# Optimization experiments

Measured on AMD Instinct MI355X. Metric: run time of the kernel, lower is better.

The kernel has to match this reference:

```python
import jax, jax.numpy as jnp
import numpy as np

V, D, L, H, T = 32000, 1024, 4, 16, 1024
DH = D // H
SCALE = DH ** -0.5
FF = 4 * D
R = 2  # n_rounds


def setup_inputs() -> dict:
    key = jax.random.key(0)
    ks = iter(jax.random.split(key, 32))
    s = 0.02
    nrm = lambda shape: jax.random.normal(next(ks), shape, dtype=jnp.float32) * s
    inp = {
        "x": jax.random.randint(next(ks), (2, T), 0, V),
        "embed": nrm((V, D)),
        "pos_embed": nrm((T, D)),
        "Wqkv": nrm((L, R, 3 * D, D)),
        "bqkv": jnp.zeros((L, R, 3 * D), jnp.float32),
        "Wo": nrm((L, D, D)),
        "bo": jnp.zeros((L, D), jnp.float32),
        "Wg": nrm((L, D, 2 * D)),
        "bg": jnp.zeros((L, D), jnp.float32),
        "ln1_g": jnp.ones((L, D), jnp.float32),
        "ln1_b": jnp.zeros((L, D), jnp.float32),
        "W1": nrm((L, FF, D)),
        "b1": jnp.zeros((L, FF), jnp.float32),
        "W2": nrm((L, D, FF)),
        "b2": jnp.zeros((L, D), jnp.float32),
        "ln2_g": jnp.ones((L, D), jnp.float32),
        "ln2_b": jnp.zeros((L, D), jnp.float32),
        "lnf_g": jnp.ones((D,), jnp.float32),
        "lnf_b": jnp.zeros((D,), jnp.float32),
    }
    return inp


def _ln(h, g, b, eps=1e-5):
    m = jnp.mean(h, axis=-1, keepdims=True)
    v = jnp.mean((h - m) ** 2, axis=-1, keepdims=True)
    return (h - m) * jax.lax.rsqrt(v + eps) * g + b


def _attend(h, W, b, mask):
    B, Tq, _ = h.shape
    qkv = (h @ W.T + b).reshape(B, Tq, 3, H, DH)
    q, k, v = qkv[:, :, 0], qkv[:, :, 1], qkv[:, :, 2]  # [B,T,H,DH]
    scores = jnp.einsum("bqhd,bkhd->bhqk", q, k) * SCALE
    scores = jnp.where(mask, scores, -jnp.inf)
    a = jax.nn.softmax(scores, axis=-1)
    return jnp.einsum("bhqk,bkhd->bqhd", a, v).reshape(B, Tq, D)


def reference(x, embed, pos_embed, Wqkv, bqkv, Wo, bo, Wg, bg,
              ln1_g, ln1_b, W1, b1, W2, b2, ln2_g, ln2_b, lnf_g, lnf_b):
    B, Tq = x.shape
    mask = jnp.tril(jnp.ones((Tq, Tq), dtype=bool))
    h = embed[x] + pos_embed[jnp.arange(Tq)]
    for l in range(L):
        n1 = _ln(h, ln1_g[l], ln1_b[l])
        pred = _attend(n1, Wqkv[l, 0], bqkv[l, 0], mask)
        cum = pred
        out = pred
        # boosted round 2: attend on residual, gate the correction
        corr = _attend(n1 - cum, Wqkv[l, 1], bqkv[l, 1], mask)
        gate = jax.nn.sigmoid(jnp.concatenate([cum, corr], axis=-1) @ Wg[l].T + bg[l])
        gated = gate * corr
        out = out + gated
        h = h + (out @ Wo[l].T + bo[l])
        n2 = _ln(h, ln2_g[l], ln2_b[l])
        ff = jax.nn.gelu(n2 @ W1[l].T + b1[l], approximate=False) @ W2[l].T + b2[l]
        h = h + ff
    return _ln(h, lnf_g, lnf_b) @ embed.T  # tied head, no bias
```

## Files before the change

### kernel.cpp

```cpp
#include <hip/hip_runtime.h>
#include <math.h>

#define D_  1024
#define T_  1024
#define B_  2
#define H_  16
#define DH_ 64
#define L_  4
#define FF_ 4096
#define V_  32000
#define M_  2048

typedef _Float16 f16;
typedef _Float16 f16x8 __attribute__((ext_vector_type(8)));
typedef _Float16 f16x4 __attribute__((ext_vector_type(4)));
typedef float    fx4  __attribute__((ext_vector_type(4)));

__global__ __launch_bounds__(256) void f2h_k(const float* __restrict__ in, f16* __restrict__ out) {
    const long i = ((long)blockIdx.x * 256 + threadIdx.x) * 4;
    const float4 v = *(const float4*)(in + i);
    f16x4 o = { (f16)v.x, (f16)v.y, (f16)v.z, (f16)v.w };
    *(f16x4*)(out + i) = o;
}

__global__ __launch_bounds__(256) void embed_k(const int* __restrict__ x, const float* __restrict__ emb,
                                               const float* __restrict__ pos, float* __restrict__ h) {
    const long m = blockIdx.x;
    const int  t = threadIdx.x;
    const long tok = x[m];
    const long pt  = m & (T_ - 1);
    const float4 e = ((const float4*)(emb + tok * D_))[t];
    const float4 p = ((const float4*)(pos + pt * D_))[t];
    ((float4*)(h + m * D_))[t] = make_float4(e.x + p.x, e.y + p.y, e.z + p.z, e.w + p.w);
}

__global__ __launch_bounds__(256) void ln_k(const float* __restrict__ x, const float* __restrict__ g,
                                            const float* __restrict__ b, float* __restrict__ of,
                                            f16* __restrict__ oh) {
    const long m = blockIdx.x;
    const int  t = threadIdx.x;
    const int  wave = t >> 6, lane = t & 63;
    __shared__ float red1[4], red2[4];
    const float4 v = ((const float4*)(x + m * D_))[t];
    float s = v.x + v.y + v.z + v.w;
#pragma unroll
    for (int off = 32; off; off >>= 1) s += __shfl_xor(s, off, 64);
    if (lane == 0) red1[wave] = s;
    __syncthreads();
    const float mean = (red1[0] + red1[1] + red1[2] + red1[3]) * (1.0f / 1024.0f);
    const float d0 = v.x - mean, d1 = v.y - mean, d2 = v.z - mean, d3 = v.w - mean;
    float s2 = d0 * d0 + d1 * d1 + d2 * d2 + d3 * d3;
#pragma unroll
    for (int off = 32; off; off >>= 1) s2 += __shfl_xor(s2, off, 64);
    if (lane == 0) red2[wave] = s2;
    __syncthreads();
    const float var  = (red2[0] + red2[1] + red2[2] + red2[3]) * (1.0f / 1024.0f);
    const float rstd = rsqrtf(var + 1e-5f);
    const float4 gv = ((const float4*)g)[t];
    const float4 bv = ((const float4*)b)[t];
    const float o0 = d0 * rstd * gv.x + bv.x;
    const float o1 = d1 * rstd * gv.y + bv.y;
    const float o2 = d2 * rstd * gv.z + bv.z;
    const float o3 = d3 * rstd * gv.w + bv.w;
    if (of) ((float4*)(of + m * D_))[t] = make_float4(o0, o1, o2, o3);
    if (oh) { f16x4 o = { (f16)o0, (f16)o1, (f16)o2, (f16)o3 }; *(f16x4*)(oh + m * D_ + t * 4) = o; }
}

__global__ __launch_bounds__(256) void sub_k(const float* __restrict__ a, const float* __restrict__ b,
                                             f16* __restrict__ o) {
    const long i = ((long)blockIdx.x * 256 + threadIdx.x) * 4;
    const float4 va = *(const float4*)(a + i);
    const float4 vb = *(const float4*)(b + i);
    f16x4 o4 = { (f16)(va.x - vb.x), (f16)(va.y - vb.y), (f16)(va.z - vb.z), (f16)(va.w - vb.w) };
    *(f16x4*)(o + i) = o4;
}

__global__ __launch_bounds__(256) void cat_k(const float* __restrict__ p, const float* __restrict__ c,
                                             f16* __restrict__ o) {
    const long i = ((long)blockIdx.x * 256 + threadIdx.x) * 4;
    const long m = i >> 11;
    const int  j = (int)(i & 2047);
    const float* src = (j < 1024) ? (p + m * 1024 + j) : (c + m * 1024 + (j - 1024));
    const float4 v = *(const float4*)src;
    f16x4 o4 = { (f16)v.x, (f16)v.y, (f16)v.z, (f16)v.w };
    *(f16x4*)(o + i) = o4;
}

__global__ __launch_bounds__(256) void gate_k(const float* __restrict__ p, const float* __restrict__ c,
                                              const float* __restrict__ gl, f16* __restrict__ o) {
    const long i = ((long)blockIdx.x * 256 + threadIdx.x) * 4;
    const float4 vp = *(const float4*)(p + i);
    const float4 vc = *(const float4*)(c + i);
    const float4 vg = *(const float4*)(gl + i);
    const float s0 = 1.0f / (1.0f + __expf(-vg.x));
    const float s1 = 1.0f / (1.0f + __expf(-vg.y));
    const float s2 = 1.0f / (1.0f + __expf(-vg.z));
    const float s3 = 1.0f / (1.0f + __expf(-vg.w));
    f16x4 o4 = { (f16)(vp.x + s0 * vc.x), (f16)(vp.y + s1 * vc.y),
                 (f16)(vp.z + s2 * vc.z), (f16)(vp.w + s3 * vc.w) };
    *(f16x4*)(o + i) = o4;
}

template<int BN>
__global__ __launch_bounds__(256)
void gemm_bt(const f16* __restrict__ A, const f16* __restrict__ Wt,
             const float* __restrict__ bias, const float* __restrict__ resid,
             float* __restrict__ Cf, f16* __restrict__ Ch,
             int N, int K, int gelu) {
    __shared__ __align__(16) f16 As[3][128 * 32];
    __shared__ __align__(16) f16 Bs[3][BN * 32];
    const int tid  = threadIdx.x;
    const int wave = tid >> 6;
    const int lane = tid & 63;

    const int nbm = gridDim.y;
    const int nbn = gridDim.x;
    int bi = blockIdx.y * nbn + blockIdx.x;
    const int nwg = nbm * nbn;
    if ((nwg & 7) == 0) bi = (bi & 7) * (nwg >> 3) + (bi >> 3);
    const long bm = bi % nbm;
    const long bn = bi / nbm;

    const int wm = (wave >> 1) * 64;
    const int wn = (wave & 1) * (BN / 2);
    constexpr int NJ = BN / 32;

    fx4 acc[4][NJ] = {};

    const int c0 = wave * 2;
    const int r0 = c0 * 16 + (lane >> 2);
    const int cc = (lane & 3) * 8;
    const f16* a0 = A + ((long)bm * 128 + r0) * K + cc;
    const f16* a1 = A + ((long)bm * 128 + r0 + 16) * K + cc;

    const f16* b0;
    const f16* b1 = nullptr;
    if constexpr (BN == 128) {
        b0 = Wt + ((long)bn * 128 + r0) * K + cc;
        b1 = Wt + ((long)bn * 128 + r0 + 16) * K + cc;
    } else {
        b0 = Wt + ((long)bn * 64 + wave * 16 + (lane >> 2)) * K + cc;
    }

    const int NT = K >> 5;

    auto STAGE = [&](int kt) {
        const int k0 = kt * 32;
        const int bf3 = kt % 3;
        __builtin_amdgcn_global_load_lds((const __attribute__((address_space(1))) void*)(a0 + k0),
                                         (__attribute__((address_space(3))) void*)&As[bf3][c0 * 512], 16, 0, 0);
        __builtin_amdgcn_global_load_lds((const __attribute__((address_space(1))) void*)(a1 + k0),
                                         (__attribute__((address_space(3))) void*)&As[bf3][(c0 + 1) * 512], 16, 0, 0);
        if constexpr (BN == 128) {
            __builtin_amdgcn_global_load_lds((const __attribute__((address_space(1))) void*)(b0 + k0),
                                             (__attribute__((address_space(3))) void*)&Bs[bf3][c0 * 512], 16, 0, 0);
            __builtin_amdgcn_global_load_lds((const __attribute__((address_space(1))) void*)(b1 + k0),
                                             (__attribute__((address_space(3))) void*)&Bs[bf3][(c0 + 1) * 512], 16, 0, 0);
        } else {
            __builtin_amdgcn_global_load_lds((const __attribute__((address_space(1))) void*)(b0 + k0),
                                             (__attribute__((address_space(3))) void*)&Bs[bf3][wave * 512], 16, 0, 0);
        }
    };

    STAGE(0);
    if (NT > 1) STAGE(1);

    const int koff = (lane >> 4) * 8;
    for (int t = 0; t < NT; ++t) {
        if (t + 2 < NT) STAGE(t + 2);
        const int rem = NT - 1 - t;
        if constexpr (BN == 128) {
            if (rem >= 2)      asm volatile("s_waitcnt vmcnt(8)" ::: "memory");
            else if (rem == 1) asm volatile("s_waitcnt vmcnt(4)" ::: "memory");
            else               asm volatile("s_waitcnt vmcnt(0)" ::: "memory");
        } else {
            if (rem >= 2)      asm volatile("s_waitcnt vmcnt(6)" ::: "memory");
            else if (rem == 1) asm volatile("s_waitcnt vmcnt(3)" ::: "memory");
            else               asm volatile("s_waitcnt vmcnt(0)" ::: "memory");
        }
        __builtin_amdgcn_s_barrier();
        __builtin_amdgcn_sched_barrier(0);

        const f16* as = As[t % 3];
        const f16* bs = Bs[t % 3];
        f16x8 af[4], bf[NJ];
#pragma unroll
        for (int i = 0; i < 4; ++i)
            af[i] = *(const f16x8*)&as[(wm + i * 16 + (lane & 15)) * 32 + koff];
#pragma unroll
        for (int j = 0; j < NJ; ++j)
            bf[j] = *(const f16x8*)&bs[(wn + j * 16 + (lane & 15)) * 32 + koff];
#pragma unroll
        for (int i = 0; i < 4; ++i)
#pragma unroll
            for (int j = 0; j < NJ; ++j)
                acc[i][j] = __builtin_amdgcn_mfma_f32_16x16x32_f16(af[i], bf[j], acc[i][j], 0, 0, 0);

        asm volatile("s_waitcnt lgkmcnt(0)" ::: "memory");
        __builtin_amdgcn_sched_barrier(0);
        __builtin_amdgcn_s_barrier();
    }

    const long gr_base = bm * 128 + wm + (lane >> 4) * 4;
    const long gc_base = bn * BN + wn + (lane & 15);
#pragma unroll
    for (int i = 0; i < 4; ++i) {
#pragma unroll
        for (int j = 0; j < NJ; ++j) {
            const long gc = gc_base + j * 16;
            const float bv = bias ? bias[gc] : 0.0f;
#pragma unroll
            for (int r = 0; r < 4; ++r) {
                const long gr = gr_base + i * 16 + r;
                float v = acc[i][j][r] + bv;
                if (gelu) v = 0.5f * v * (1.0f + erff(v * 0.70710678118654752f));
                else if (resid) v += resid[gr * (long)N + gc];
                if (Cf) Cf[gr * (long)N + gc] = v;
                if (Ch) Ch[gr * (long)N + gc] = (f16)v;
            }
        }
    }
}

__global__ __launch_bounds__(256) void fattn_k(const f16* __restrict__ qkv, float* __restrict__ out) {
    __shared__ __align__(16) f16 Ks[64 * 72];
    __shared__ __align__(16) f16 Vt[64 * 72];
    __shared__ __align__(16) f16 Pw[4][16 * 72];
    const int tid  = threadIdx.x;
    const int w    = tid >> 6;
    const int lane = tid & 63;
    const int b  = blockIdx.z, h = blockIdx.y;
    const int qt = (gridDim.x - 1) - blockIdx.x;
    const int q0w = qt * 64 + w * 16;
    const int g  = lane >> 4;
    const int lm = lane & 15;

    const long qrow = ((long)(b * T_ + q0w + lm)) * (3 * D_) + h * DH_;
    f16x8 af_q[2];
    af_q[0] = *(const f16x8*)(qkv + qrow + g * 8);
    af_q[1] = *(const f16x8*)(qkv + qrow + 32 + g * 8);

    float m_r[4], l_r[4];
    fx4 acc_o[4] = {};
#pragma unroll
    for (int r = 0; r < 4; ++r) { m_r[r] = -INFINITY; l_r[r] = 0.0f; }

    const int srow = tid >> 2;
    const int scol = (tid & 3) * 16;
    const long kbase = ((long)(b * T_)) * (3 * D_) + D_ + h * DH_ + scol;
    const long vbase = kbase + D_;

    const int nkb = qt + 1;
    for (int it = 0; it < nkb; ++it) {
        const int kb = it * 64;
        __syncthreads();
        {
            const f16* ksrc = qkv + kbase + (long)(kb + srow) * (3 * D_);
            f16x8 k0 = *(const f16x8*)(ksrc);
            f16x8 k1 = *(const f16x8*)(ksrc + 8);
            *(f16x8*)&Ks[srow * 72 + scol]     = k0;
            *(f16x8*)&Ks[srow * 72 + scol + 8] = k1;
            const f16* vsrc = qkv + vbase + (long)(kb + srow) * (3 * D_);
            f16x8 v0 = *(const f16x8*)(vsrc);
            f16x8 v1 = *(const f16x8*)(vsrc + 8);
#pragma unroll
            for (int i = 0; i < 8; ++i) {
                const int d = scol + i;
                Vt[d * 72 + (srow ^ (((d >> 2) & 7) << 3))] = v0[i];
            }
#pragma unroll
            for (int i = 0; i < 8; ++i) {
                const int d = scol + 8 + i;
                Vt[d * 72 + (srow ^ (((d >> 2) & 7) << 3))] = v1[i];
            }
        }
        __syncthreads();

        fx4 sc[4];
#pragma unroll
        for (int kt = 0; kt < 4; ++kt) {
            fx4 c = {};
#pragma unroll
            for (int kk = 0; kk < 2; ++kk) {
                f16x8 bf = *(const f16x8*)&Ks[(kt * 16 + lm) * 72 + kk * 32 + g * 8];
                c = __builtin_amdgcn_mfma_f32_16x16x32_f16(af_q[kk], bf, c, 0, 0, 0);
            }
            sc[kt] = c * 0.125f;
        }
        if (kb == qt * 64) {
#pragma unroll
            for (int kt = 0; kt < 4; ++kt) {
                const int key_g = kb + kt * 16 + lm;
#pragma unroll
                for (int r = 0; r < 4; ++r)
                    if (key_g > q0w + g * 4 + r) sc[kt][r] = -INFINITY;
            }
        }

        float mnew[4], pscale[4];
#pragma unroll
        for (int r = 0; r < 4; ++r) {
            float tm = fmaxf(fmaxf(sc[0][r], sc[1][r]), fmaxf(sc[2][r], sc[3][r]));
#pragma unroll
            for (int off = 8; off; off >>= 1) tm = fmaxf(tm, __shfl_xor(tm, off, 64));
            mnew[r]   = fmaxf(m_r[r], tm);
            pscale[r] = __expf(m_r[r] - mnew[r]);
        }
        float psum[4] = {};
#pragma unroll
        for (int kt = 0; kt < 4; ++kt) {
#pragma unroll
            for (int r = 0; r < 4; ++r) {
                const float p = __expf(sc[kt][r] - mnew[r]);
                sc[kt][r] = p;
                psum[r] += p;
            }
        }
#pragma unroll
        for (int r = 0; r < 4; ++r) {
#pragma unroll
            for (int off = 8; off; off >>= 1) psum[r] += __shfl_xor(psum[r], off, 64);
            l_r[r] = l_r[r] * pscale[r] + psum[r];
            m_r[r] = mnew[r];
        }
#pragma unroll
        for (int nt = 0; nt < 4; ++nt)
#pragma unroll
            for (int r = 0; r < 4; ++r) acc_o[nt][r] *= pscale[r];

        f16* P = Pw[w];
#pragma unroll
        for (int kt = 0; kt < 4; ++kt)
#pragma unroll
            for (int r = 0; r < 4; ++r)
                P[(g * 4 + r) * 72 + kt * 16 + lm] = (f16)sc[kt][r];

#pragma unroll
        for (int kc = 0; kc < 2; ++kc) {
            f16x8 ap = *(const f16x8*)&P[lm * 72 + kc * 32 + g * 8];
#pragma unroll
            for (int nt = 0; nt < 4; ++nt) {
                const int d = nt * 16 + lm;
                const int col = (kc * 32 + g * 8) ^ (((d >> 2) & 7) << 3);
                f16x8 bv = *(const f16x8*)&Vt[d * 72 + col];
                acc_o[nt] = __builtin_amdgcn_mfma_f32_16x16x32_f16(ap, bv, acc_o[nt], 0, 0, 0);
            }
        }
    }

    const long obase = ((long)(b * T_ + q0w + g * 4)) * D_ + h * DH_ + lm;
#pragma unroll
    for (int r = 0; r < 4; ++r) {
        const float inv = 1.0f / l_r[r];
#pragma unroll
        for (int nt = 0; nt < 4; ++nt)
            out[obase + (long)r * D_ + nt * 16] = acc_o[nt][r] * inv;
    }
}

extern "C" void kernel_launch(void* const* d_in, const int* in_sizes, int n_in,
                              void* d_out, int out_size, void* d_ws, size_t ws_size,
                              hipStream_t stream) {
    const int*   x    = (const int*)d_in[0];
    const float* emb  = (const float*)d_in[1];
    const float* pos  = (const float*)d_in[2];
    const float* Wqkv = (const float*)d_in[3];
    const float* bqkv = (const float*)d_in[4];
    const float* Wo   = (const float*)d_in[5];
    const float* bo   = (const float*)d_in[6];
    const float* Wg   = (const float*)d_in[7];
    const float* bg   = (const float*)d_in[8];
    const float* ln1g = (const float*)d_in[9];
    const float* ln1b = (const float*)d_in[10];
    const float* W1   = (const float*)d_in[11];
    const float* b1   = (const float*)d_in[12];
    const float* W2   = (const float*)d_in[13];
    const float* b2   = (const float*)d_in[14];
    const float* ln2g = (const float*)d_in[15];
    const float* ln2b = (const float*)d_in[16];
    const float* lnfg = (const float*)d_in[17];
    const float* lnfb = (const float*)d_in[18];
    float* out = (float*)d_out;

    char* ws = (char*)d_ws;
    size_t off = 0;
    auto alloc = [&](size_t bytes) -> void* {
        off = (off + 255) & ~(size_t)255;
        void* p = ws + off;
        off += bytes;
        return p;
    };
    float* h    = (float*)alloc((size_t)M_ * D_ * 4);
    float* n1f  = (float*)alloc((size_t)M_ * D_ * 4);
    float* pred = (float*)alloc((size_t)M_ * D_ * 4);
    float* corr = (float*)alloc((size_t)M_ * D_ * 4);
    float* glin = (float*)alloc((size_t)M_ * D_ * 4);
    f16* qkvh  = (f16*)alloc((size_t)M_ * 3 * D_ * 2);
    f16* ab    = (f16*)alloc((size_t)M_ * D_ * 2);
    f16* catb  = (f16*)alloc((size_t)M_ * 2 * D_ * 2);
    f16* ffh   = (f16*)alloc((size_t)M_ * FF_ * 2);
    f16* embh  = (f16*)alloc((size_t)V_ * D_ * 2);
    f16* wqkvh = (f16*)alloc((size_t)L_ * 2 * 3 * D_ * D_ * 2);
    f16* woh   = (f16*)alloc((size_t)L_ * D_ * D_ * 2);
    f16* wgh   = (f16*)alloc((size_t)L_ * D_ * 2 * D_ * 2);
    f16* w1h   = (f16*)alloc((size_t)L_ * FF_ * D_ * 2);
    f16* w2h   = (f16*)alloc((size_t)L_ * D_ * FF_ * 2);

    auto cvt = [&](const float* src, f16* dst, long n) {
        f2h_k<<<dim3((unsigned)(n / 1024)), dim3(256), 0, stream>>>(src, dst);
    };
    cvt(emb,  embh,  (long)V_ * D_);
    cvt(Wqkv, wqkvh, (long)L_ * 2 * 3 * D_ * D_);
    cvt(Wo,   woh,   (long)L_ * D_ * D_);
    cvt(Wg,   wgh,   (long)L_ * D_ * 2 * D_);
    cvt(W1,   w1h,   (long)L_ * FF_ * D_);
    cvt(W2,   w2h,   (long)L_ * D_ * FF_);

    embed_k<<<dim3(M_), dim3(256), 0, stream>>>(x, emb, pos, h);

    auto gemm = [&](const f16* A, const f16* Wt, const float* bias, const float* resid,
                    float* Cf, f16* Ch, int N, int K, int gelu) {
        if (N <= 1024)
            gemm_bt<64><<<dim3(N / 64, M_ / 128), dim3(256), 0, stream>>>(A, Wt, bias, resid, Cf, Ch, N, K, gelu);
        else
            gemm_bt<128><<<dim3(N / 128, M_ / 128), dim3(256), 0, stream>>>(A, Wt, bias, resid, Cf, Ch, N, K, gelu);
    };

    for (int l = 0; l < L_; ++l) {
        ln_k<<<dim3(M_), 256, 0, stream>>>(h, ln1g + l * D_, ln1b + l * D_, n1f, ab);
        gemm(ab, wqkvh + (size_t)(l * 2 + 0) * 3 * D_ * D_, bqkv + (l * 2 + 0) * 3 * D_,
             nullptr, nullptr, qkvh, 3 * D_, D_, 0);
        fattn_k<<<dim3(T_ / 64, H_, B_), 256, 0, stream>>>(qkvh, pred);
        sub_k<<<dim3(M_ * D_ / 1024), 256, 0, stream>>>(n1f, pred, ab);
        gemm(ab, wqkvh + (size_t)(l * 2 + 1) * 3 * D_ * D_, bqkv + (l * 2 + 1) * 3 * D_,
             nullptr, nullptr, qkvh, 3 * D_, D_, 0);
        fattn_k<<<dim3(T_ / 64, H_, B_), 256, 0, stream>>>(qkvh, corr);
        cat_k<<<dim3(M_ * 2 * D_ / 1024), 256, 0, stream>>>(pred, corr, catb);
        gemm(catb, wgh + (size_t)l * D_ * 2 * D_, bg + l * D_, nullptr, glin, nullptr, D_, 2 * D_, 0);
        gate_k<<<dim3(M_ * D_ / 1024), 256, 0, stream>>>(pred, corr, glin, ab);
        gemm(ab, woh + (size_t)l * D_ * D_, bo + l * D_, h, h, nullptr, D_, D_, 0);
        ln_k<<<dim3(M_), 256, 0, stream>>>(h, ln2g + l * D_, ln2b + l * D_, nullptr, ab);
        gemm(ab, w1h + (size_t)l * FF_ * D_, b1 + l * FF_, nullptr, nullptr, ffh, FF_, D_, 1);
        gemm(ffh, w2h + (size_t)l * D_ * FF_, b2 + l * D_, h, h, nullptr, D_, FF_, 0);
    }
    ln_k<<<dim3(M_), 256, 0, stream>>>(h, lnfg, lnfb, nullptr, ab);
    gemm(ab, embh, nullptr, nullptr, out, nullptr, V_, D_, 0);
}
```

Measured before the change: 2.295 ms.

## Swizzle GEMM LDS layout and prefetch attention K/V tiles into registers

The GEMM kernel now XOR-swizzles the k-chunk offset used when staging A/B tiles into LDS and when reading them back for MFMA, to reduce LDS bank conflicts. In the attention kernel, the next K/V block is loaded into registers while the current block is being computed, so global latency overlaps with MFMA work. The transposed V store is also reorganised so each thread writes two adjacent keys as one packed f16x2 instead of scalar halves. The costs are more registers held across the loop and a swizzle that must match exactly between the global_load_lds writes and the fragment reads.

```diff
diff --git a/kernel.cpp b/kernel.cpp
--- a/kernel.cpp
+++ b/kernel.cpp
@@ -14,6 +14,7 @@
 typedef _Float16 f16;
 typedef _Float16 f16x8 __attribute__((ext_vector_type(8)));
 typedef _Float16 f16x4 __attribute__((ext_vector_type(4)));
+typedef _Float16 f16x2 __attribute__((ext_vector_type(2)));
 typedef float    fx4  __attribute__((ext_vector_type(4)));
 
 __global__ __launch_bounds__(256) void f2h_k(const float* __restrict__ in, f16* __restrict__ out) {
@@ -129,7 +130,7 @@
 
     const int c0 = wave * 2;
     const int r0 = c0 * 16 + (lane >> 2);
-    const int cc = (lane & 3) * 8;
+    const int cc = ((lane & 3) ^ ((lane >> 3) & 3)) * 8;
     const f16* a0 = A + ((long)bm * 128 + r0) * K + cc;
     const f16* a1 = A + ((long)bm * 128 + r0 + 16) * K + cc;
 
@@ -165,7 +166,9 @@
     STAGE(0);
     if (NT > 1) STAGE(1);
 
-    const int koff = (lane >> 4) * 8;
+    const int lm = lane & 15;
+    const int g  = lane >> 4;
+    const int koff = (g ^ ((lm >> 1) & 3)) * 8;
     for (int t = 0; t < NT; ++t) {
         if (t + 2 < NT) STAGE(t + 2);
         const int rem = NT - 1 - t;
@@ -186,10 +189,10 @@
         f16x8 af[4], bf[NJ];
 #pragma unroll
         for (int i = 0; i < 4; ++i)
-            af[i] = *(const f16x8*)&as[(wm + i * 16 + (lane & 15)) * 32 + koff];
+            af[i] = *(const f16x8*)&as[(wm + i * 16 + lm) * 32 + koff];
 #pragma unroll
         for (int j = 0; j < NJ; ++j)
-            bf[j] = *(const f16x8*)&bs[(wn + j * 16 + (lane & 15)) * 32 + koff];
+            bf[j] = *(const f16x8*)&bs[(wn + j * 16 + lm) * 32 + koff];
 #pragma unroll
         for (int i = 0; i < 4; ++i)
 #pragma unroll
@@ -248,33 +251,44 @@
     const int srow = tid >> 2;
     const int scol = (tid & 3) * 16;
     const long kbase = ((long)(b * T_)) * (3 * D_) + D_ + h * DH_ + scol;
-    const long vbase = kbase + D_;
+    const int vm  = tid >> 3;
+    const int vd0 = (tid & 7) * 8;
+    const long vbase = ((long)(b * T_)) * (3 * D_) + 2 * D_ + h * DH_ + vd0;
+
+    f16x8 kr0, kr1, vr0, vr1;
+    {
+        const f16* ks = qkv + kbase + (long)srow * (3 * D_);
+        kr0 = *(const f16x8*)(ks);
+        kr1 = *(const f16x8*)(ks + 8);
+        const f16* va = qkv + vbase + (long)(2 * vm) * (3 * D_);
+        vr0 = *(const f16x8*)(va);
+        vr1 = *(const f16x8*)(va + 3 * D_);
+    }
 
     const int nkb = qt + 1;
     for (int it = 0; it < nkb; ++it) {
         const int kb = it * 64;
         __syncthreads();
-        {
-            const f16* ksrc = qkv + kbase + (long)(kb + srow) * (3 * D_);
-            f16x8 k0 = *(const f16x8*)(ksrc);
-            f16x8 k1 = *(const f16x8*)(ksrc + 8);
-            *(f16x8*)&Ks[srow * 72 + scol]     = k0;
-            *(f16x8*)&Ks[srow * 72 + scol + 8] = k1;
-            const f16* vsrc = qkv + vbase + (long)(kb + srow) * (3 * D_);
-            f16x8 v0 = *(const f16x8*)(vsrc);
-            f16x8 v1 = *(const f16x8*)(vsrc + 8);
-#pragma unroll
-            for (int i = 0; i < 8; ++i) {
-                const int d = scol + i;
-                Vt[d * 72 + (srow ^ (((d >> 2) & 7) << 3))] = v0[i];
-            }
-#pragma unroll
-            for (int i = 0; i < 8; ++i) {
-                const int d = scol + 8 + i;
-                Vt[d * 72 + (srow ^ (((d >> 2) & 7) << 3))] = v1[i];
-            }
+        *(f16x8*)&Ks[srow * 72 + scol]     = kr0;
+        *(f16x8*)&Ks[srow * 72 + scol + 8] = kr1;
+#pragma unroll
+        for (int j = 0; j < 8; ++j) {
+            const int d = vd0 + j;
+            const int col = (2 * vm) ^ (((d >> 2) & 7) << 3);
+            f16x2 pr = { vr0[j], vr1[j] };
+            *(f16x2*)&Vt[d * 72 + col] = pr;
         }
         __syncthreads();
+
+        if (it + 1 < nkb) {
+            const int kb2 = kb + 64;
+            const f16* ks = qkv + kbase + (long)(kb2 + srow) * (3 * D_);
+            kr0 = *(const f16x8*)(ks);
+            kr1 = *(const f16x8*)(ks + 8);
+            const f16* va = qkv + vbase + (long)(kb2 + 2 * vm) * (3 * D_);
+            vr0 = *(const f16x8*)(va);
+            vr1 = *(const f16x8*)(va + 3 * D_);
+        }
 
         fx4 sc[4];
 #pragma unroll
```

Result: faster. 2.200 ms (-4.1%).
